# Kernel optimization log

Measured on AMD Instinct MI355X. Metric: run time of the kernel, lower is better.

The kernel has to match this reference:

```python
import jax, jax.numpy as jnp
import numpy as np

EPS = 1e-5

def conv3x3(x, W, b):
    # NCHW 3x3 conv, padding=1 (SAME)
    y = jax.lax.conv_general_dilated(x, W, (1, 1), ((1, 1), (1, 1)),
                                     dimension_numbers=('NCHW', 'OIHW', 'NCHW'))
    return y + b[None, :, None, None]

def bn_relu(x, gamma, beta):
    # BatchNorm2d in training mode: batch statistics over (N,H,W)
    m = x.mean(axis=(0, 2, 3), keepdims=True)
    v = x.var(axis=(0, 2, 3), keepdims=True)
    xn = (x - m) * jax.lax.rsqrt(v + EPS)
    return jax.nn.relu(xn * gamma[None, :, None, None] + beta[None, :, None, None])

def haar_dwt2(x):
    # pywt.dwt2(x, 'db1') for even H,W: cA=LL, cH=row-detail/col-approx,
    # cV=row-approx/col-detail, cD=HH; each 0.5*(+-a +-b +-c +-d)
    a = x[:, :, 0::2, 0::2]
    b = x[:, :, 0::2, 1::2]
    c = x[:, :, 1::2, 0::2]
    d = x[:, :, 1::2, 1::2]
    cA = (a + b + c + d) * 0.5
    cH = (a + b - c - d) * 0.5
    cV = (a - b + c - d) * 0.5
    cD = (a - b - c + d) * 0.5
    return jnp.concatenate([cA, cH, cV, cD], axis=1)  # [B, 4C, H/2, W/2]

def setup_inputs() -> dict:
    key = jax.random.key(0)
    ks = jax.random.split(key, 4)
    B, Cin, Cout, H, W = 8, 64, 128, 256, 256
    inputs = jax.random.normal(ks[0], (B, Cin, H, W), dtype=jnp.float32)
    W1 = jax.random.normal(ks[1], (Cout, Cin, 3, 3), dtype=jnp.float32) * 0.05
    W2 = jax.random.normal(ks[2], (Cout, Cout, 3, 3), dtype=jnp.float32) * 0.05
    W3 = jax.random.normal(ks[3], (Cout, 4 * Cout, 3, 3), dtype=jnp.float32) * 0.05
    z = jnp.zeros((Cout,), jnp.float32)
    o = jnp.ones((Cout,), jnp.float32)
    return {"inputs": inputs,
            "W1": W1, "b1": z, "g1": o, "be1": z,
            "W2": W2, "b2": z, "g2": o, "be2": z,
            "W3": W3, "b3": z, "g3": o, "be3": z}

def reference(inputs, W1, b1, g1, be1, W2, b2, g2, be2, W3, b3, g3, be3):
    h = bn_relu(conv3x3(inputs, W1, b1), g1, be1)
    skip_con = bn_relu(conv3x3(h, W2, b2), g2, be2)          # [B, out_c, H, W]
    # original detaches before the pywt round-trip
    dwt = haar_dwt2(jax.lax.stop_gradient(skip_con))          # [B, 4*out_c, H/2, W/2]
    dwt_out = bn_relu(conv3x3(dwt, W3, b3), g3, be3)          # [B, out_c, H/2, W/2]
    return (skip_con, dwt_out)
```

## Files before the change

kernel.cpp:

```cpp
#include <hip/hip_runtime.h>

typedef __attribute__((ext_vector_type(8))) short bf16x8;
typedef __attribute__((ext_vector_type(4))) short bf16x4;
typedef __attribute__((ext_vector_type(4))) float f32x4;

__device__ __forceinline__ float bf2f(ushort u) {
  union { unsigned int i; float f; } v; v.i = ((unsigned int)u) << 16; return v.f;
}
__device__ __forceinline__ ushort f2bf(float f) {
  union { float f; unsigned int i; } v; v.f = f;
  unsigned int x = v.i;
  unsigned int r = (x + 0x7fffu + ((x >> 16) & 1u)) >> 16;
  return (ushort)r;
}

__global__ void zero_f32(float* p, int n) {
  int i = blockIdx.x * 256 + threadIdx.x;
  if (i < n) p[i] = 0.f;
}

__global__ void pack_w(const float* __restrict__ W, ushort* __restrict__ Wp, int Cin) {
  int ncic = Cin >> 5;
  int total = ncic * 4 * 64 * 9 * 2 * 8;
  for (int idx = blockIdx.x * 256 + threadIdx.x; idx < total; idx += gridDim.x * 256) {
    int j = idx & 7;
    int f = (idx >> 3) & 1;
    int rest = idx >> 4;
    int tap = rest % 9;  rest /= 9;
    int l = rest & 63;
    int pc = rest >> 6;
    int pair = pc & 3;
    int cic = pc >> 2;
    int co = ((pair << 1) | f) * 16 + (l & 15);
    int ci = (cic << 5) + ((l >> 4) << 3) + j;
    int ky = tap / 3, kx = tap % 3;
    Wp[idx] = f2bf(W[((co * Cin + ci) * 3 + ky) * 3 + kx]);
  }
}

__global__ __launch_bounds__(256)
void nchw2nhwc(const float* __restrict__ in, ushort* __restrict__ out) {
  const int n  = blockIdx.y;
  const int p0 = blockIdx.x << 6;
  const int tid = threadIdx.x;
  __shared__ ushort t[64 * 72];
  {
    int c  = tid >> 2;
    int pq = (tid & 3) << 4;
    const float* ip = in + (((size_t)(n * 64 + c)) << 16) + p0 + pq;
#pragma unroll
    for (int k = 0; k < 4; ++k) {
      float4 f = *(const float4*)(ip + k * 4);
      int p = pq + k * 4;
      t[(p + 0) * 72 + c] = f2bf(f.x);
      t[(p + 1) * 72 + c] = f2bf(f.y);
      t[(p + 2) * 72 + c] = f2bf(f.z);
      t[(p + 3) * 72 + c] = f2bf(f.w);
    }
  }
  __syncthreads();
#pragma unroll
  for (int k = 0; k < 2; ++k) {
    int id = k * 256 + tid;
    int cj = id & 7, p = id >> 3;
    bf16x8 v = *(const bf16x8*)&t[p * 72 + cj * 8];
    *(bf16x8*)(out + ((((size_t)n << 16) + p0 + p) << 6) + cj * 8) = v;
  }
}

__device__ __forceinline__ bf16x8 bnrelu8(bf16x8 v, const float* __restrict__ coef, int c0) {
  float4 a0 = *(const float4*)(coef + c0);
  float4 a1 = *(const float4*)(coef + c0 + 4);
  float4 b0 = *(const float4*)(coef + 128 + c0);
  float4 b1 = *(const float4*)(coef + 128 + c0 + 4);
  bf16x8 r;
  r[0] = (short)f2bf(fmaxf(a0.x * bf2f((ushort)v[0]) + b0.x, 0.f));
  r[1] = (short)f2bf(fmaxf(a0.y * bf2f((ushort)v[1]) + b0.y, 0.f));
  r[2] = (short)f2bf(fmaxf(a0.z * bf2f((ushort)v[2]) + b0.z, 0.f));
  r[3] = (short)f2bf(fmaxf(a0.w * bf2f((ushort)v[3]) + b0.w, 0.f));
  r[4] = (short)f2bf(fmaxf(a1.x * bf2f((ushort)v[4]) + b1.x, 0.f));
  r[5] = (short)f2bf(fmaxf(a1.y * bf2f((ushort)v[5]) + b1.y, 0.f));
  r[6] = (short)f2bf(fmaxf(a1.z * bf2f((ushort)v[6]) + b1.z, 0.f));
  r[7] = (short)f2bf(fmaxf(a1.w * bf2f((ushort)v[7]) + b1.w, 0.f));
  return r;
}

template<int MODE>
__global__ __launch_bounds__(256)
void conv_mfma(const ushort* __restrict__ src, const ushort* __restrict__ Wp,
               const float* __restrict__ bias, const float* __restrict__ coef,
               ushort* __restrict__ out, float* __restrict__ sSum, float* __restrict__ sSsq,
               int Cin, int H, int W)
{
  const int ncic = Cin >> 5;
  const int x0 = blockIdx.x << 6;
  const int y0 = blockIdx.y << 1;
  const int n  = blockIdx.z;
  const int tid = threadIdx.x;
  const int wv = tid >> 6, l = tid & 63, l15 = l & 15, l4 = l >> 4;

  __shared__ __align__(16) char smem[17408];
  ushort* lds = (ushort*)smem;
  ushort* eps = (ushort*)smem;

  f32x4 acc[2][2][4];
#pragma unroll
  for (int yr = 0; yr < 2; ++yr)
#pragma unroll
    for (int f = 0; f < 2; ++f)
#pragma unroll
      for (int xf = 0; xf < 4; ++xf) acc[yr][f][xf] = (f32x4){0.f, 0.f, 0.f, 0.f};

  const size_t HW = (size_t)H * W;

  for (int cic = 0; cic < ncic; ++cic) {
    __syncthreads();
    for (int i = tid; i < 1056; i += 256) {
      int cj = i & 3;
      int t = i >> 2;
      int row = t / 66;
      int xt = t - row * 66;
      int ry = y0 + row - 1;
      int gx = x0 + xt - 1;
      bf16x8 v = {};
      if ((unsigned)ry < (unsigned)H && (unsigned)gx < (unsigned)W) {
        const ushort* p = src + ((size_t)n * HW + (size_t)ry * W + gx) * Cin + (cic << 5) + (cj << 3);
        v = *(const bf16x8*)p;
        if (MODE == 1) v = bnrelu8(v, coef, (cic << 5) + (cj << 3));
      }
      *(bf16x8*)&lds[(((row << 2) | cj) * 66 + xt) << 3] = v;
    }
    __syncthreads();

    const ushort* wp = Wp + (((size_t)(cic * 4 + wv) * 64 + l) * 144);

#pragma unroll
    for (int tap = 0; tap < 9; ++tap) {
      const int ky = tap / 3, kx = tap % 3;
      bf16x8 afr[2];
#pragma unroll
      for (int f = 0; f < 2; ++f)
        afr[f] = *(const bf16x8*)(wp + (tap * 2 + f) * 8);
      bf16x8 bfr[2][4];
#pragma unroll
      for (int yr = 0; yr < 2; ++yr)
#pragma unroll
        for (int xf = 0; xf < 4; ++xf) {
          int row = yr + ky;
          int xt = (xf << 4) + l15 + kx;
          bfr[yr][xf] = *(const bf16x8*)&lds[(((row << 2) | l4) * 66 + xt) << 3];
        }
#pragma unroll
      for (int f = 0; f < 2; ++f)
#pragma unroll
        for (int yr = 0; yr < 2; ++yr)
#pragma unroll
          for (int xf = 0; xf < 4; ++xf)
            acc[yr][f][xf] = __builtin_amdgcn_mfma_f32_16x16x32_bf16(afr[f], bfr[yr][xf], acc[yr][f][xf], 0, 0, 0);
    }
  }

  float sm[2][4] = {{0.f}}, sq[2][4] = {{0.f}};
  const int cb = (wv << 5) + (l4 << 2);
  for (int yr = 0; yr < 2; ++yr) {
    __syncthreads();
#pragma unroll
    for (int f = 0; f < 2; ++f) {
      const int cf = cb + (f << 4);
      float4 bv = *(const float4*)(bias + cf);
#pragma unroll
      for (int xf = 0; xf < 4; ++xf) {
        float v0 = acc[yr][f][xf][0] + bv.x;
        float v1 = acc[yr][f][xf][1] + bv.y;
        float v2 = acc[yr][f][xf][2] + bv.z;
        float v3 = acc[yr][f][xf][3] + bv.w;
        sm[f][0] += v0; sq[f][0] += v0 * v0;
        sm[f][1] += v1; sq[f][1] += v1 * v1;
        sm[f][2] += v2; sq[f][2] += v2 * v2;
        sm[f][3] += v3; sq[f][3] += v3 * v3;
        bf16x4 u;
        u[0] = (short)f2bf(v0); u[1] = (short)f2bf(v1);
        u[2] = (short)f2bf(v2); u[3] = (short)f2bf(v3);
        *(bf16x4*)&eps[((xf << 4) + l15) * 136 + cf] = u;
      }
    }
    __syncthreads();
    {
      const int xx = tid >> 2, c0 = (tid & 3) << 5;
      ushort* op = out + ((size_t)n * HW + (size_t)(y0 + yr) * W + x0 + xx) * 128 + c0;
#pragma unroll
      for (int k = 0; k < 4; ++k)
        *(bf16x8*)(op + (k << 3)) = *(const bf16x8*)&eps[xx * 136 + c0 + (k << 3)];
    }
  }

  const int rep = (int)((blockIdx.z * gridDim.y + blockIdx.y) * gridDim.x + blockIdx.x) & 31;
#pragma unroll
  for (int f = 0; f < 2; ++f)
#pragma unroll
    for (int j = 0; j < 4; ++j) {
      float s = sm[f][j], q = sq[f][j];
#pragma unroll
      for (int o = 1; o < 16; o <<= 1) { s += __shfl_xor(s, o); q += __shfl_xor(q, o); }
      if (l15 == 0) {
        int co = cb + (f << 4) + j;
        atomicAdd(&sSum[rep * 128 + co], s);
        atomicAdd(&sSsq[rep * 128 + co], q);
      }
    }
}

__global__ void bn_finalize(const float* __restrict__ sSum, const float* __restrict__ sSsq,
                            const float* __restrict__ g, const float* __restrict__ be,
                            float* __restrict__ coef, float invN)
{
  int c = threadIdx.x;
  float S = 0.f, Q = 0.f;
  for (int r = 0; r < 32; ++r) { S += sSum[r * 128 + c]; Q += sSsq[r * 128 + c]; }
  float m = S * invN;
  float v = Q * invN - m * m;
  float a = g[c] / sqrtf(v + 1e-5f);
  coef[c] = a;
  coef[128 + c] = be[c] - m * a;
}

__global__ __launch_bounds__(256)
void skip_dwt2(const ushort* __restrict__ skipRaw, const float* __restrict__ coef,
               float* __restrict__ outSkip, ushort* __restrict__ dwt)
{
  const int x0 = blockIdx.x << 6;
  const int oy = blockIdx.y;
  const int n  = blockIdx.z >> 2;
  const int ct = blockIdx.z & 3;
  const int y0 = oy << 1;
  const int tid = threadIdx.x;
  __shared__ float t32[32 * 2 * 68];

#pragma unroll
  for (int it = 0; it < 2; ++it) {
    int i = it * 256 + tid;
    int cj = i & 3, x = (i >> 2) & 63, r = i >> 8;
    int c0 = (ct << 5) + (cj << 3);
    bf16x8 v = *(const bf16x8*)(skipRaw + (((size_t)n << 16) + (size_t)(y0 + r) * 256 + x0 + x) * 128 + c0);
    float4 a0 = *(const float4*)(coef + c0);
    float4 a1 = *(const float4*)(coef + c0 + 4);
    float4 b0 = *(const float4*)(coef + 128 + c0);
    float4 b1 = *(const float4*)(coef + 128 + c0 + 4);
    float av[8] = {a0.x, a0.y, a0.z, a0.w, a1.x, a1.y, a1.z, a1.w};
    float bv[8] = {b0.x, b0.y, b0.z, b0.w, b1.x, b1.y, b1.z, b1.w};
    int cl = cj << 3;
#pragma unroll
    for (int k = 0; k < 8; ++k)
      t32[((cl + k) * 2 + r) * 68 + x] = fmaxf(av[k] * bf2f((ushort)v[k]) + bv[k], 0.f);
  }
  __syncthreads();

  {
    int c = tid >> 3, x8 = (tid & 7) << 3;
    float* op = outSkip + (((size_t)(n * 128 + (ct << 5) + c)) << 16) + (size_t)y0 * 256 + x0 + x8;
#pragma unroll
    for (int r = 0; r < 2; ++r) {
      float4 r0 = *(const float4*)&t32[(c * 2 + r) * 68 + x8];
      float4 r1 = *(const float4*)&t32[(c * 2 + r) * 68 + x8 + 4];
      *(float4*)(op + (size_t)r * 256) = r0;
      *(float4*)(op + (size_t)r * 256 + 4) = r1;
    }
  }

  if (tid < 128) {
    int cj = tid & 3, ox = tid >> 2;
    int cl = cj << 3;
    bf16x8 oA, oH, oV, oD;
#pragma unroll
    for (int k = 0; k < 8; ++k) {
      int c = cl + k;
      float p00 = t32[(c * 2 + 0) * 68 + 2 * ox];
      float p01 = t32[(c * 2 + 0) * 68 + 2 * ox + 1];
      float p10 = t32[(c * 2 + 1) * 68 + 2 * ox];
      float p11 = t32[(c * 2 + 1) * 68 + 2 * ox + 1];
      oA[k] = (short)f2bf((p00 + p01 + p10 + p11) * 0.5f);
      oH[k] = (short)f2bf((p00 + p01 - p10 - p11) * 0.5f);
      oV[k] = (short)f2bf((p00 - p01 + p10 - p11) * 0.5f);
      oD[k] = (short)f2bf((p00 - p01 - p10 + p11) * 0.5f);
    }
    size_t db = ((size_t)n * 16384 + (size_t)oy * 128 + (x0 >> 1) + ox) * 512 + (ct << 5) + cl;
    *(bf16x8*)(dwt + db)       = oA;
    *(bf16x8*)(dwt + db + 128) = oH;
    *(bf16x8*)(dwt + db + 256) = oV;
    *(bf16x8*)(dwt + db + 384) = oD;
  }
}

__global__ __launch_bounds__(256)
void bn_transpose_out(const ushort* __restrict__ src, const float* __restrict__ coef,
                      float* __restrict__ dst, int H, int W)
{
  const int n  = blockIdx.z >> 2;
  const int cc = blockIdx.z & 3;
  const int x0 = blockIdx.x << 6;
  const int y  = blockIdx.y;
  const int tid = threadIdx.x;
  __shared__ float t[32 * 68];
  const size_t HW = (size_t)H * W;
  {
    int p = tid >> 2, cj = tid & 3;
    int c0 = (cc << 5) + (cj << 3);
    bf16x8 v = *(const bf16x8*)(src + ((size_t)n * HW + (size_t)y * W + x0 + p) * 128 + c0);
    float4 a0 = *(const float4*)(coef + c0);
    float4 a1 = *(const float4*)(coef + c0 + 4);
    float4 b0 = *(const float4*)(coef + 128 + c0);
    float4 b1 = *(const float4*)(coef + 128 + c0 + 4);
    int cl = cj << 3;
    t[(cl + 0) * 68 + p] = fmaxf(a0.x * bf2f((ushort)v[0]) + b0.x, 0.f);
    t[(cl + 1) * 68 + p] = fmaxf(a0.y * bf2f((ushort)v[1]) + b0.y, 0.f);
    t[(cl + 2) * 68 + p] = fmaxf(a0.z * bf2f((ushort)v[2]) + b0.z, 0.f);
    t[(cl + 3) * 68 + p] = fmaxf(a0.w * bf2f((ushort)v[3]) + b0.w, 0.f);
    t[(cl + 4) * 68 + p] = fmaxf(a1.x * bf2f((ushort)v[4]) + b1.x, 0.f);
    t[(cl + 5) * 68 + p] = fmaxf(a1.y * bf2f((ushort)v[5]) + b1.y, 0.f);
    t[(cl + 6) * 68 + p] = fmaxf(a1.z * bf2f((ushort)v[6]) + b1.z, 0.f);
    t[(cl + 7) * 68 + p] = fmaxf(a1.w * bf2f((ushort)v[7]) + b1.w, 0.f);
  }
  __syncthreads();
  {
    int c = tid >> 3, x8 = (tid & 7) << 3;
    float4 r0 = *(const float4*)&t[c * 68 + x8];
    float4 r1 = *(const float4*)&t[c * 68 + x8 + 4];
    float* op = dst + ((size_t)(n * 128 + (cc << 5) + c)) * HW + (size_t)y * W + x0 + x8;
    *(float4*)op = r0;
    *(float4*)(op + 4) = r1;
  }
}

extern "C" void kernel_launch(void* const* d_in, const int* in_sizes, int n_in,
                              void* d_out, int out_size, void* d_ws, size_t ws_size,
                              hipStream_t stream)
{
  const float* input = (const float*)d_in[0];
  const float* W1  = (const float*)d_in[1];
  const float* b1  = (const float*)d_in[2];
  const float* g1  = (const float*)d_in[3];
  const float* be1 = (const float*)d_in[4];
  const float* W2  = (const float*)d_in[5];
  const float* b2  = (const float*)d_in[6];
  const float* g2  = (const float*)d_in[7];
  const float* be2 = (const float*)d_in[8];
  const float* W3  = (const float*)d_in[9];
  const float* b3  = (const float*)d_in[10];
  const float* g3  = (const float*)d_in[11];
  const float* be3 = (const float*)d_in[12];

  char* ws = (char*)d_ws;
  ushort* h_raw    = (ushort*)(ws + 0);
  ushort* skip_raw = (ushort*)(ws + 134217728);
  ushort* dwt      = (ushort*)(ws + 268435456);
  ushort* in_nhwc  = (ushort*)(ws + 268435456);
  ushort* raw3     = (ushort*)(ws + 402653184);
  float*  stats    = (float*)(ws + 436207616);
  float*  s1 = stats,          *q1 = stats + 4096;
  float*  s2 = stats + 8192,   *q2 = stats + 12288;
  float*  s3 = stats + 16384,  *q3 = stats + 20480;
  float*  coef = (float*)(ws + 436305920);
  float*  c1 = coef, *c2 = coef + 256, *c3 = coef + 512;
  ushort* Wp1 = (ushort*)(ws + 436308992);
  ushort* Wp2 = (ushort*)(ws + 436456448);
  ushort* Wp3 = (ushort*)(ws + 436751360);

  zero_f32<<<96, 256, 0, stream>>>(stats, 24576);
  pack_w<<<288, 256, 0, stream>>>(W1, Wp1, 64);
  pack_w<<<576, 256, 0, stream>>>(W2, Wp2, 128);
  pack_w<<<2304, 256, 0, stream>>>(W3, Wp3, 512);
  nchw2nhwc<<<dim3(1024, 8), 256, 0, stream>>>(input, in_nhwc);

  conv_mfma<0><<<dim3(4, 128, 8), 256, 0, stream>>>(in_nhwc, Wp1, b1, nullptr,
                                                    h_raw, s1, q1, 64, 256, 256);
  bn_finalize<<<1, 128, 0, stream>>>(s1, q1, g1, be1, c1, 1.f / 524288.f);

  conv_mfma<1><<<dim3(4, 128, 8), 256, 0, stream>>>(h_raw, Wp2, b2, c1,
                                                    skip_raw, s2, q2, 128, 256, 256);
  bn_finalize<<<1, 128, 0, stream>>>(s2, q2, g2, be2, c2, 1.f / 524288.f);

  skip_dwt2<<<dim3(4, 128, 32), 256, 0, stream>>>(skip_raw, c2, (float*)d_out, dwt);

  conv_mfma<0><<<dim3(2, 64, 8), 256, 0, stream>>>(dwt, Wp3, b3, nullptr,
                                                   raw3, s3, q3, 512, 128, 128);
  bn_finalize<<<1, 128, 0, stream>>>(s3, q3, g3, be3, c3, 1.f / 131072.f);

  bn_transpose_out<<<dim3(2, 128, 32), 256, 0, stream>>>(raw3, c3, (float*)d_out + 67108864, 128, 128);
}
```

Baseline: 847.8 us.

## Remap conv waves to 2 channel groups × 2 rows with repacked weights

Changes the wave-to-work mapping in the MFMA conv so each wave computes 64 output channels for one output row, instead of 32 channels across both rows. The weight packing is reordered to a tap-major, cic, channel-fragment layout so each wave loads four A fragments per tap from a contiguous stride. This halves the LDS B-fragment reads per MFMA, since four A fragments are reused against four B fragments, at the cost of more global weight fragment loads per wave. The epilogue is restructured so only the waves owning the current row write to the staging buffer, which leaves half the waves idle in each row pass.

```diff
diff --git a/kernel.cpp b/kernel.cpp
--- a/kernel.cpp
+++ b/kernel.cpp
@@ -21,18 +21,16 @@
 
 __global__ void pack_w(const float* __restrict__ W, ushort* __restrict__ Wp, int Cin) {
   int ncic = Cin >> 5;
-  int total = ncic * 4 * 64 * 9 * 2 * 8;
+  int total = 9 * ncic * 8 * 64 * 8;
   for (int idx = blockIdx.x * 256 + threadIdx.x; idx < total; idx += gridDim.x * 256) {
     int j = idx & 7;
-    int f = (idx >> 3) & 1;
-    int rest = idx >> 4;
-    int tap = rest % 9;  rest /= 9;
-    int l = rest & 63;
-    int pc = rest >> 6;
-    int pair = pc & 3;
-    int cic = pc >> 2;
-    int co = ((pair << 1) | f) * 16 + (l & 15);
-    int ci = (cic << 5) + ((l >> 4) << 3) + j;
+    int l = (idx >> 3) & 63;
+    int cf = (idx >> 9) & 7;
+    int rest = idx >> 12;
+    int cic = rest % ncic;
+    int tap = rest / ncic;
+    int co = cf * 16 + (l & 15);
+    int ci = cic * 32 + ((l >> 4) * 8) + j;
     int ky = tap / 3, kx = tap % 3;
     Wp[idx] = f2bf(W[((co * Cin + ci) * 3 + ky) * 3 + kx]);
   }
@@ -98,18 +96,18 @@
   const int n  = blockIdx.z;
   const int tid = threadIdx.x;
   const int wv = tid >> 6, l = tid & 63, l15 = l & 15, l4 = l >> 4;
+  const int cg = wv >> 1;
+  const int wy = wv & 1;
 
   __shared__ __align__(16) char smem[17408];
   ushort* lds = (ushort*)smem;
   ushort* eps = (ushort*)smem;
 
-  f32x4 acc[2][2][4];
-#pragma unroll
-  for (int yr = 0; yr < 2; ++yr)
-#pragma unroll
-    for (int f = 0; f < 2; ++f)
-#pragma unroll
-      for (int xf = 0; xf < 4; ++xf) acc[yr][f][xf] = (f32x4){0.f, 0.f, 0.f, 0.f};
+  f32x4 acc[4][4];
+#pragma unroll
+  for (int f = 0; f < 4; ++f)
+#pragma unroll
+    for (int xf = 0; xf < 4; ++xf) acc[f][xf] = (f32x4){0.f, 0.f, 0.f, 0.f};
 
   const size_t HW = (size_t)H * W;
 
@@ -132,56 +130,54 @@
     }
     __syncthreads();
 
-    const ushort* wp = Wp + (((size_t)(cic * 4 + wv) * 64 + l) * 144);
+    const ushort* wp = Wp + (((size_t)cic * 8) + (cg << 2)) * 512 + ((size_t)l << 3);
+    const size_t tstride = (size_t)ncic * 4096;
 
 #pragma unroll
     for (int tap = 0; tap < 9; ++tap) {
       const int ky = tap / 3, kx = tap % 3;
-      bf16x8 afr[2];
-#pragma unroll
-      for (int f = 0; f < 2; ++f)
-        afr[f] = *(const bf16x8*)(wp + (tap * 2 + f) * 8);
-      bf16x8 bfr[2][4];
-#pragma unroll
-      for (int yr = 0; yr < 2; ++yr)
-#pragma unroll
-        for (int xf = 0; xf < 4; ++xf) {
-          int row = yr + ky;
-          int xt = (xf << 4) + l15 + kx;
-          bfr[yr][xf] = *(const bf16x8*)&lds[(((row << 2) | l4) * 66 + xt) << 3];
-        }
-#pragma unroll
-      for (int f = 0; f < 2; ++f)
-#pragma unroll
-        for (int yr = 0; yr < 2; ++yr)
-#pragma unroll
-          for (int xf = 0; xf < 4; ++xf)
-            acc[yr][f][xf] = __builtin_amdgcn_mfma_f32_16x16x32_bf16(afr[f], bfr[yr][xf], acc[yr][f][xf], 0, 0, 0);
-    }
-  }
-
-  float sm[2][4] = {{0.f}}, sq[2][4] = {{0.f}};
-  const int cb = (wv << 5) + (l4 << 2);
+      bf16x8 afr[4];
+#pragma unroll
+      for (int f = 0; f < 4; ++f)
+        afr[f] = *(const bf16x8*)(wp + (size_t)tap * tstride + (f << 9));
+      bf16x8 bfr[4];
+#pragma unroll
+      for (int xf = 0; xf < 4; ++xf) {
+        int row = wy + ky;
+        int xt = (xf << 4) + l15 + kx;
+        bfr[xf] = *(const bf16x8*)&lds[(((row << 2) | l4) * 66 + xt) << 3];
+      }
+#pragma unroll
+      for (int f = 0; f < 4; ++f)
+#pragma unroll
+        for (int xf = 0; xf < 4; ++xf)
+          acc[f][xf] = __builtin_amdgcn_mfma_f32_16x16x32_bf16(afr[f], bfr[xf], acc[f][xf], 0, 0, 0);
+    }
+  }
+
+  float sm[4][4] = {{0.f}}, sq[4][4] = {{0.f}};
   for (int yr = 0; yr < 2; ++yr) {
     __syncthreads();
-#pragma unroll
-    for (int f = 0; f < 2; ++f) {
-      const int cf = cb + (f << 4);
-      float4 bv = *(const float4*)(bias + cf);
-#pragma unroll
-      for (int xf = 0; xf < 4; ++xf) {
-        float v0 = acc[yr][f][xf][0] + bv.x;
-        float v1 = acc[yr][f][xf][1] + bv.y;
-        float v2 = acc[yr][f][xf][2] + bv.z;
-        float v3 = acc[yr][f][xf][3] + bv.w;
-        sm[f][0] += v0; sq[f][0] += v0 * v0;
-        sm[f][1] += v1; sq[f][1] += v1 * v1;
-        sm[f][2] += v2; sq[f][2] += v2 * v2;
-        sm[f][3] += v3; sq[f][3] += v3 * v3;
-        bf16x4 u;
-        u[0] = (short)f2bf(v0); u[1] = (short)f2bf(v1);
-        u[2] = (short)f2bf(v2); u[3] = (short)f2bf(v3);
-        *(bf16x4*)&eps[((xf << 4) + l15) * 136 + cf] = u;
+    if (wy == yr) {
+#pragma unroll
+      for (int f = 0; f < 4; ++f) {
+        const int col = (cg << 6) + (f << 4) + (l4 << 2);
+        float4 bv = *(const float4*)(bias + col);
+#pragma unroll
+        for (int xf = 0; xf < 4; ++xf) {
+          float v0 = acc[f][xf][0] + bv.x;
+          float v1 = acc[f][xf][1] + bv.y;
+          float v2 = acc[f][xf][2] + bv.z;
+          float v3 = acc[f][xf][3] + bv.w;
+          sm[f][0] += v0; sq[f][0] += v0 * v0;
+          sm[f][1] += v1; sq[f][1] += v1 * v1;
+          sm[f][2] += v2; sq[f][2] += v2 * v2;
+          sm[f][3] += v3; sq[f][3] += v3 * v3;
+          bf16x4 u;
+          u[0] = (short)f2bf(v0); u[1] = (short)f2bf(v1);
+          u[2] = (short)f2bf(v2); u[3] = (short)f2bf(v3);
+          *(bf16x4*)&eps[((xf << 4) + l15) * 136 + col] = u;
+        }
       }
     }
     __syncthreads();
@@ -196,14 +192,14 @@
 
   const int rep = (int)((blockIdx.z * gridDim.y + blockIdx.y) * gridDim.x + blockIdx.x) & 31;
 #pragma unroll
-  for (int f = 0; f < 2; ++f)
+  for (int f = 0; f < 4; ++f)
 #pragma unroll
     for (int j = 0; j < 4; ++j) {
       float s = sm[f][j], q = sq[f][j];
 #pragma unroll
       for (int o = 1; o < 16; o <<= 1) { s += __shfl_xor(s, o); q += __shfl_xor(q, o); }
       if (l15 == 0) {
-        int co = cb + (f << 4) + j;
+        int co = (cg << 6) + (f << 4) + (l4 << 2) + j;
         atomicAdd(&sSum[rep * 128 + co], s);
         atomicAdd(&sSsq[rep * 128 + co], q);
       }
```

Measured after the change: 1.023 ms. 20.7% more time.

## Reorder packed weight layout for coalesced loads and precompute halo load offsets

Applied to the files above, without the earlier changes.

Changes the packed weight layout so that for each tap and channel chunk, the 64 lanes read contiguous 16-byte fragments, making per-wave weight loads coalesced instead of strided by 144 elements. The halo tile load loop is unrolled into five fixed iterations with per-thread global offsets and LDS destinations precomputed once outside the channel-chunk loop. This removes repeated integer division and bounds checks from the inner loop, at the cost of ten extra registers per thread.

```diff
diff --git a/kernel.cpp b/kernel.cpp
--- a/kernel.cpp
+++ b/kernel.cpp
@@ -21,18 +21,16 @@
 
 __global__ void pack_w(const float* __restrict__ W, ushort* __restrict__ Wp, int Cin) {
   int ncic = Cin >> 5;
-  int total = ncic * 4 * 64 * 9 * 2 * 8;
+  int total = 9 * ncic * 8 * 64 * 8;
   for (int idx = blockIdx.x * 256 + threadIdx.x; idx < total; idx += gridDim.x * 256) {
     int j = idx & 7;
-    int f = (idx >> 3) & 1;
-    int rest = idx >> 4;
-    int tap = rest % 9;  rest /= 9;
-    int l = rest & 63;
-    int pc = rest >> 6;
-    int pair = pc & 3;
-    int cic = pc >> 2;
-    int co = ((pair << 1) | f) * 16 + (l & 15);
-    int ci = (cic << 5) + ((l >> 4) << 3) + j;
+    int l = (idx >> 3) & 63;
+    int cf = (idx >> 9) & 7;
+    int rest = idx >> 12;
+    int cic = rest % ncic;
+    int tap = rest / ncic;
+    int co = cf * 16 + (l & 15);
+    int ci = cic * 32 + ((l >> 4) * 8) + j;
     int ky = tap / 3, kx = tap % 3;
     Wp[idx] = f2bf(W[((co * Cin + ci) * 3 + ky) * 3 + kx]);
   }
@@ -112,27 +110,38 @@
       for (int xf = 0; xf < 4; ++xf) acc[yr][f][xf] = (f32x4){0.f, 0.f, 0.f, 0.f};
 
   const size_t HW = (size_t)H * W;
+  const ushort* srcn = src + (size_t)n * HW * Cin;
+  const int cjc = (tid & 3) << 3;
+
+  int off[5], wch[5];
+#pragma unroll
+  for (int it = 0; it < 5; ++it) {
+    int i = it * 256 + tid;
+    int cj = i & 3, p = i >> 2;
+    int row = p / 66, xt = p - row * 66;
+    int ry = y0 + row - 1, gx = x0 + xt - 1;
+    bool ok = (i < 1056) && ((unsigned)ry < (unsigned)H) && ((unsigned)gx < (unsigned)W);
+    off[it] = ok ? (int)((ry * W + gx) * Cin + (cj << 3)) : -1;
+    wch[it] = ((row << 2) | cj) * 66 + xt;
+  }
 
   for (int cic = 0; cic < ncic; ++cic) {
     __syncthreads();
-    for (int i = tid; i < 1056; i += 256) {
-      int cj = i & 3;
-      int t = i >> 2;
-      int row = t / 66;
-      int xt = t - row * 66;
-      int ry = y0 + row - 1;
-      int gx = x0 + xt - 1;
-      bf16x8 v = {};
-      if ((unsigned)ry < (unsigned)H && (unsigned)gx < (unsigned)W) {
-        const ushort* p = src + ((size_t)n * HW + (size_t)ry * W + gx) * Cin + (cic << 5) + (cj << 3);
-        v = *(const bf16x8*)p;
-        if (MODE == 1) v = bnrelu8(v, coef, (cic << 5) + (cj << 3));
+#pragma unroll
+    for (int it = 0; it < 5; ++it) {
+      if (it < 4 || tid < 32) {
+        bf16x8 v = {};
+        if (off[it] >= 0) {
+          v = *(const bf16x8*)(srcn + off[it] + (cic << 5));
+          if (MODE == 1) v = bnrelu8(v, coef, (cic << 5) + cjc);
+        }
+        *(bf16x8*)&lds[wch[it] << 3] = v;
       }
-      *(bf16x8*)&lds[(((row << 2) | cj) * 66 + xt) << 3] = v;
     }
     __syncthreads();
 
-    const ushort* wp = Wp + (((size_t)(cic * 4 + wv) * 64 + l) * 144);
+    const ushort* wp = Wp + (((size_t)cic * 8) + (wv << 1)) * 512 + ((size_t)l << 3);
+    const size_t tstride = (size_t)ncic * 4096;
 
 #pragma unroll
     for (int tap = 0; tap < 9; ++tap) {
@@ -140,7 +149,7 @@
       bf16x8 afr[2];
 #pragma unroll
       for (int f = 0; f < 2; ++f)
-        afr[f] = *(const bf16x8*)(wp + (tap * 2 + f) * 8);
+        afr[f] = *(const bf16x8*)(wp + (size_t)tap * tstride + (f << 9));
       bf16x8 bfr[2][4];
 #pragma unroll
       for (int yr = 0; yr < 2; ++yr)
```

Result: faster. 765.0 us (-9.8%).
